# Kernel optimization log

Measured on AMD Instinct MI355X. Metric: run time of the kernel, lower is better.

The kernel has to match this reference:

```python
import jax, jax.numpy as jnp
import numpy as np

LABEL_SMOOTHING = 0.1


def setup_inputs() -> dict:
    key = jax.random.key(0)
    k1, k2, k3 = jax.random.split(key, 3)
    B, N, D = 16384, 1000, 1000  # code structurally requires D == n_classes == N
    inputs = jax.random.uniform(k1, (B, D), dtype=jnp.float32)
    labels = jax.random.randint(k2, (B,), 0, N, dtype=jnp.int64)
    code_book = jax.random.uniform(k3, (N, D), dtype=jnp.float32)
    return {"inputs": inputs, "labels": labels, "code_book": code_book}


def reference(inputs, labels, code_book):
    # inputs: [B, D], code_book: [N, D], D == N (n_classes)
    n_classes = inputs.shape[1]
    # soft targets with label smoothing (same as scatter_ + smoothing)
    soft_target = jax.nn.one_hot(labels, n_classes, dtype=inputs.dtype)
    soft_target = soft_target * (1.0 - LABEL_SMOOTHING) + LABEL_SMOOTHING / n_classes
    # Hamming similarity: sum_d [o*c + (1-o)*(1-c)]  ==  o@c.T + (1-o)@(1-c).T
    # (algebraic rewrite of the [B, N, D] broadcast in the original; same math)
    similarity = (jnp.einsum("bd,nd->bn", inputs, code_book)
                  + jnp.einsum("bd,nd->bn", 1.0 - inputs, 1.0 - code_book))
    logp = jax.nn.log_softmax(similarity, axis=1)
    return jnp.mean(jnp.sum(-soft_target * logp, axis=1))
```

## Files before the change

kernel.cpp:

```cpp
#include <hip/hip_runtime.h>

typedef __attribute__((ext_vector_type(8))) short bf16x8;
typedef __attribute__((ext_vector_type(4))) float f32x4;

#define AS1 __attribute__((address_space(1)))
#define AS3 __attribute__((address_space(3)))

__device__ static inline void gl2lds16(const void* g, void* l) {
  __builtin_amdgcn_global_load_lds((const AS1 unsigned int*)g, (AS3 unsigned int*)l, 16, 0, 0);
}

__device__ static inline unsigned short f2bf(float x) {
  unsigned int u = __float_as_uint(x);
  unsigned int r = u + 0x7FFFu + ((u >> 16) & 1u);
  return (unsigned short)(r >> 16);
}

__global__ __launch_bounds__(256) void prep_inputs_k(const float* __restrict__ in,
                                                     unsigned short* __restrict__ a) {
  int idx = blockIdx.x * 256 + threadIdx.x;
  int row = idx >> 7;
  int g   = idx & 127;
  union { unsigned short u[8]; uint4 v; } pk;
  if (g < 125) {
    const float4* p = (const float4*)(in + (size_t)row * 1000 + g * 8);
    float4 v0 = p[0], v1 = p[1];
    pk.u[0] = f2bf(2.f * v0.x); pk.u[1] = f2bf(2.f * v0.y);
    pk.u[2] = f2bf(2.f * v0.z); pk.u[3] = f2bf(2.f * v0.w);
    pk.u[4] = f2bf(2.f * v1.x); pk.u[5] = f2bf(2.f * v1.y);
    pk.u[6] = f2bf(2.f * v1.z); pk.u[7] = f2bf(2.f * v1.w);
  } else {
    pk.v = make_uint4(0, 0, 0, 0);
  }
  *(uint4*)(a + ((size_t)row << 10) + (g << 3)) = pk.v;
}

__global__ __launch_bounds__(256) void prep_code_k(const float* __restrict__ cb,
                                                   unsigned short* __restrict__ b,
                                                   float* __restrict__ rowsum) {
  int n = blockIdx.x;
  int t = threadIdx.x;
  float s = 0.f;
#pragma unroll
  for (int j = 0; j < 4; ++j) {
    int c = t + j * 256;
    float v = 0.f;
    if (n < 1000 && c < 1000) v = cb[(size_t)n * 1000 + c];
    s += v;
    b[((size_t)n << 10) + c] = f2bf(v);
  }
  __shared__ float red[256];
  red[t] = s;
  __syncthreads();
  for (int o = 128; o > 0; o >>= 1) {
    if (t < o) red[t] += red[t + o];
    __syncthreads();
  }
  if (t == 0) rowsum[n] = (n < 1000) ? red[0] : 0.f;
}

__global__ __launch_bounds__(256) void fix_labels_k(const int* __restrict__ raw,
                                                    int* __restrict__ labs) {
  __shared__ int nz;
  int t = threadIdx.x;
  if (t == 0) nz = 0;
  __syncthreads();
  if (raw[2 * t + 1] != 0) atomicAdd(&nz, 1);
  __syncthreads();
  bool is64 = (nz < 32);
  int row = blockIdx.x * 256 + t;
  labs[row] = is64 ? raw[2 * row] : raw[row];
}

__global__ __launch_bounds__(256, 2) void coding_loss_k(
    const unsigned short* __restrict__ A,
    const unsigned short* __restrict__ B,
    const float* __restrict__ rowsum,
    const int* __restrict__ labels,
    float* __restrict__ Z,
    float* __restrict__ lin) {
  __shared__ __align__(16) unsigned char lds[24576 + 32768 + 1040];
  unsigned short* Ab0 = (unsigned short*)lds;
  unsigned short* Ab1 = Ab0 + 4096;
  unsigned short* Ab2 = Ab1 + 4096;
  unsigned short* Bb0 = Ab2 + 4096;
  unsigned short* Bb1 = Bb0 + 8192;
  float* zbuf = (float*)(lds + 57344);
  float* lbuf = zbuf + 256;

  const int t    = threadIdx.x;
  const int lane = t & 63;
  const int w    = t >> 6;
  const int wr   = w >> 1;
  const int wc   = w & 1;
  const int g16  = lane >> 4;
  const int c16  = lane & 15;
  const int ct   = blockIdx.x & 3;
  const int rt   = blockIdx.x >> 2;
  const int r0   = rt << 7;
  const int c0   = ct << 8;

  size_t a_src[2]; int a_dst[2];
#pragma unroll
  for (int i = 0; i < 2; ++i) {
    int ch = i * 256 + t, row = ch >> 2;
    int sg = (ch & 3) ^ ((row >> 1) & 3);
    a_src[i] = (size_t)(r0 + row) * 1024 + sg * 8;
    a_dst[i] = ch * 8;
  }
  size_t b_src[4]; int b_dst[4];
#pragma unroll
  for (int i = 0; i < 4; ++i) {
    int ch = i * 256 + t, row = ch >> 2;
    int sg = (ch & 3) ^ ((row >> 1) & 3);
    b_src[i] = (size_t)(c0 + row) * 1024 + sg * 8;
    b_dst[i] = ch * 8;
  }

  int a_eoff[4], b_eoff[8];
#pragma unroll
  for (int mi = 0; mi < 4; ++mi) {
    int ar = wr * 64 + mi * 16 + c16;
    a_eoff[mi] = ar * 32 + ((g16 ^ ((ar >> 1) & 3)) << 3);
  }
#pragma unroll
  for (int ni = 0; ni < 8; ++ni) {
    int br = wc * 128 + ni * 16 + c16;
    b_eoff[ni] = br * 32 + ((g16 ^ ((br >> 1) & 3)) << 3);
  }

  f32x4 acc[4][8];
#pragma unroll
  for (int mi = 0; mi < 4; ++mi)
#pragma unroll
    for (int ni = 0; ni < 8; ++ni) acc[mi][ni] = (f32x4)(0.f);

#define STAGE_A(kk, dst) \
  { _Pragma("unroll") for (int i = 0; i < 2; ++i) gl2lds16(A + a_src[i] + (kk) * 32, (dst) + a_dst[i]); }
#define STAGE_B(kk, dst) \
  { _Pragma("unroll") for (int i = 0; i < 4; ++i) gl2lds16(B + b_src[i] + (kk) * 32, (dst) + b_dst[i]); }
#define COMPUTE(pa, pb)                                                                   \
  {                                                                                       \
    bf16x8 af[4], bf[8];                                                                  \
    _Pragma("unroll") for (int mi = 0; mi < 4; ++mi) af[mi] = *(const bf16x8*)((pa) + a_eoff[mi]); \
    _Pragma("unroll") for (int ni = 0; ni < 8; ++ni) bf[ni] = *(const bf16x8*)((pb) + b_eoff[ni]); \
    _Pragma("unroll") for (int mi = 0; mi < 4; ++mi)                                      \
      _Pragma("unroll") for (int ni = 0; ni < 8; ++ni)                                    \
        acc[mi][ni] = __builtin_amdgcn_mfma_f32_16x16x32_bf16(af[mi], bf[ni], acc[mi][ni], 0, 0, 0); \
  }
#define WAITVM(n) __builtin_amdgcn_s_waitcnt(0xF70 | (n))

  STAGE_A(0, Ab0);
  STAGE_B(0, Bb0);
  STAGE_A(1, Ab1);

  unsigned short *pa_cur = Ab0, *pa_nxt = Ab1, *pa_stg = Ab2;
  unsigned short *pb_cur = Bb0, *pb_stg = Bb1;

#pragma unroll 2
  for (int kc = 0; kc < 30; ++kc) {
    STAGE_B(kc + 1, pb_stg);
    STAGE_A(kc + 2, pa_stg);
    WAITVM(8);
    __builtin_amdgcn_s_barrier();
    COMPUTE(pa_cur, pb_cur);
    __builtin_amdgcn_s_barrier();
    unsigned short* tmp = pa_cur; pa_cur = pa_nxt; pa_nxt = pa_stg; pa_stg = tmp;
    tmp = pb_cur; pb_cur = pb_stg; pb_stg = tmp;
  }
  {
    STAGE_B(31, pb_stg);
    WAITVM(6);
    __builtin_amdgcn_s_barrier();
    COMPUTE(pa_cur, pb_cur);
    __builtin_amdgcn_s_barrier();
    unsigned short* tmp = pa_cur; pa_cur = pa_nxt; pa_nxt = tmp;
    tmp = pb_cur; pb_cur = pb_stg; pb_stg = tmp;
  }
  {
    WAITVM(0);
    __builtin_amdgcn_s_barrier();
    COMPUTE(pa_cur, pb_cur);
  }

  float rs[8]; int colg[8];
#pragma unroll
  for (int ni = 0; ni < 8; ++ni) {
    colg[ni] = c0 + wc * 128 + ni * 16 + c16;
    rs[ni]   = rowsum[colg[ni]];
  }
  float lacc = 0.f;
  float ez[4][4];
#pragma unroll
  for (int mi = 0; mi < 4; ++mi)
#pragma unroll
    for (int r = 0; r < 4; ++r) {
      int labv = labels[r0 + wr * 64 + mi * 16 + g16 * 4 + r];
      float e = 0.f;
#pragma unroll
      for (int ni = 0; ni < 8; ++ni) {
        float S = acc[mi][ni][r] - rs[ni];
        e += __expf(S - 40.f);
        lacc += 1e-4f * S;
        if (colg[ni] == labv) lacc += 0.9f * S;
      }
      ez[mi][r] = e;
    }
#pragma unroll
  for (int d = 1; d < 16; d <<= 1)
#pragma unroll
    for (int mi = 0; mi < 4; ++mi)
#pragma unroll
      for (int r = 0; r < 4; ++r) ez[mi][r] += __shfl_xor(ez[mi][r], d, 64);
  if (c16 == 0) {
#pragma unroll
    for (int mi = 0; mi < 4; ++mi)
#pragma unroll
      for (int r = 0; r < 4; ++r) zbuf[w * 64 + mi * 16 + g16 * 4 + r] = ez[mi][r];
  }
#pragma unroll
  for (int d = 1; d < 64; d <<= 1) lacc += __shfl_xor(lacc, d, 64);
  if (lane == 0) lbuf[w] = lacc;
  __syncthreads();
  if (t < 128) {
    int wrg = t >> 6, lr = t & 63;
    float z = zbuf[(wrg * 2 + 0) * 64 + lr] + zbuf[(wrg * 2 + 1) * 64 + lr];
    Z[ct * 16384 + r0 + t] = z;
  }
  if (t == 0) atomicAdd(lin, lbuf[0] + lbuf[1] + lbuf[2] + lbuf[3]);
#undef STAGE_A
#undef STAGE_B
#undef COMPUTE
#undef WAITVM
}

__global__ __launch_bounds__(256) void finalize_k(const float* __restrict__ Z,
                                                  const float* __restrict__ lin,
                                                  float* __restrict__ out) {
  int t = threadIdx.x;
  int row = blockIdx.x * 256 + t;
  float v = 40.f + logf(Z[row] + Z[16384 + row] + Z[2 * 16384 + row] + Z[3 * 16384 + row]);
#pragma unroll
  for (int d = 1; d < 64; d <<= 1) v += __shfl_xor(v, d, 64);
  __shared__ float s[4];
  if ((t & 63) == 0) s[t >> 6] = v;
  __syncthreads();
  if (t == 0) {
    float tot = s[0] + s[1] + s[2] + s[3];
    if (blockIdx.x == 0) tot -= lin[0];
    atomicAdd(out, tot * (1.f / 16384.f));
  }
}

extern "C" void kernel_launch(void* const* d_in, const int* in_sizes, int n_in,
                              void* d_out, int out_size, void* d_ws, size_t ws_size,
                              hipStream_t stream) {
  const float* inputs = (const float*)d_in[0];
  const int* labraw   = (const int*)d_in[1];
  const float* code   = (const float*)d_in[2];

  unsigned short* a_bf = (unsigned short*)d_ws;
  unsigned short* b_bf = a_bf + (size_t)16384 * 1024;
  float* rowsum        = (float*)(b_bf + (size_t)1024 * 1024);
  float* Z             = rowsum + 1024;
  float* lin           = Z + 4 * 16384;
  int* labs            = (int*)(lin + 1);

  hipMemsetAsync(lin, 0, sizeof(float), stream);
  hipMemsetAsync(d_out, 0, sizeof(float), stream);
  fix_labels_k<<<64, 256, 0, stream>>>(labraw, labs);
  prep_inputs_k<<<8192, 256, 0, stream>>>(inputs, a_bf);
  prep_code_k<<<1024, 256, 0, stream>>>(code, b_bf, rowsum);
  coding_loss_k<<<512, 256, 0, stream>>>(a_bf, b_bf, rowsum, labs, Z, lin);
  finalize_k<<<64, 256, 0, stream>>>(Z, lin, (float*)d_out);
}
```

Before: 148.5 us.

## Merge prep kernels and enlarge GEMM tile to 256x256 with double buffering

The three preprocessing kernels and two memsets are merged into a single launch that dispatches on block index, which cuts launch overhead. The main GEMM tile grows from 128x256 to 256x256 per block, giving 8x8 MFMA accumulators per wave and more operand reuse. The 3-stage A pipeline is replaced by plain double buffering with occupancy 1 and 256 blocks. The risks are higher register pressure, only 256 blocks on a GPU with about 256 CUs leaving no latency hiding across blocks, and a shallower prefetch.

```diff
diff --git a/kernel.cpp b/kernel.cpp
--- a/kernel.cpp
+++ b/kernel.cpp
@@ -16,77 +16,71 @@
   return (unsigned short)(r >> 16);
 }
 
-__global__ __launch_bounds__(256) void prep_inputs_k(const float* __restrict__ in,
-                                                     unsigned short* __restrict__ a) {
-  int idx = blockIdx.x * 256 + threadIdx.x;
-  int row = idx >> 7;
-  int g   = idx & 127;
-  union { unsigned short u[8]; uint4 v; } pk;
-  if (g < 125) {
-    const float4* p = (const float4*)(in + (size_t)row * 1000 + g * 8);
-    float4 v0 = p[0], v1 = p[1];
-    pk.u[0] = f2bf(2.f * v0.x); pk.u[1] = f2bf(2.f * v0.y);
-    pk.u[2] = f2bf(2.f * v0.z); pk.u[3] = f2bf(2.f * v0.w);
-    pk.u[4] = f2bf(2.f * v1.x); pk.u[5] = f2bf(2.f * v1.y);
-    pk.u[6] = f2bf(2.f * v1.z); pk.u[7] = f2bf(2.f * v1.w);
+__global__ __launch_bounds__(256) void prep_all_k(
+    const float* __restrict__ in, const int* __restrict__ labraw,
+    const float* __restrict__ cb, unsigned short* __restrict__ a,
+    unsigned short* __restrict__ b, float* __restrict__ rowsum,
+    int* __restrict__ labs, float* __restrict__ lin, float* __restrict__ out) {
+  const int bx = blockIdx.x, t = threadIdx.x;
+  if (bx < 8192) {
+    int idx = bx * 256 + t;
+    int row = idx >> 7, g = idx & 127;
+    union { unsigned short u[8]; uint4 v; } pk;
+    if (g < 125) {
+      const float4* p = (const float4*)(in + (size_t)row * 1000 + g * 8);
+      float4 v0 = p[0], v1 = p[1];
+      pk.u[0] = f2bf(2.f * v0.x); pk.u[1] = f2bf(2.f * v0.y);
+      pk.u[2] = f2bf(2.f * v0.z); pk.u[3] = f2bf(2.f * v0.w);
+      pk.u[4] = f2bf(2.f * v1.x); pk.u[5] = f2bf(2.f * v1.y);
+      pk.u[6] = f2bf(2.f * v1.z); pk.u[7] = f2bf(2.f * v1.w);
+    } else {
+      pk.v = make_uint4(0, 0, 0, 0);
+    }
+    *(uint4*)(a + ((size_t)row << 10) + (g << 3)) = pk.v;
+  } else if (bx < 9216) {
+    int n = bx - 8192;
+    float s = 0.f;
+#pragma unroll
+    for (int j = 0; j < 4; ++j) {
+      int c = t + j * 256;
+      float v = 0.f;
+      if (n < 1000 && c < 1000) v = cb[(size_t)n * 1000 + c];
+      s += v;
+      b[((size_t)n << 10) + c] = f2bf(v);
+    }
+    __shared__ float red[256];
+    red[t] = s;
+    __syncthreads();
+    for (int o = 128; o > 0; o >>= 1) {
+      if (t < o) red[t] += red[t + o];
+      __syncthreads();
+    }
+    if (t == 0) rowsum[n] = (n < 1000) ? red[0] : 0.f;
   } else {
-    pk.v = make_uint4(0, 0, 0, 0);
-  }
-  *(uint4*)(a + ((size_t)row << 10) + (g << 3)) = pk.v;
-}
-
-__global__ __launch_bounds__(256) void prep_code_k(const float* __restrict__ cb,
-                                                   unsigned short* __restrict__ b,
-                                                   float* __restrict__ rowsum) {
-  int n = blockIdx.x;
-  int t = threadIdx.x;
-  float s = 0.f;
-#pragma unroll
-  for (int j = 0; j < 4; ++j) {
-    int c = t + j * 256;
-    float v = 0.f;
-    if (n < 1000 && c < 1000) v = cb[(size_t)n * 1000 + c];
-    s += v;
-    b[((size_t)n << 10) + c] = f2bf(v);
-  }
-  __shared__ float red[256];
-  red[t] = s;
-  __syncthreads();
-  for (int o = 128; o > 0; o >>= 1) {
-    if (t < o) red[t] += red[t + o];
+    __shared__ int nz;
+    if (t == 0) nz = 0;
     __syncthreads();
-  }
-  if (t == 0) rowsum[n] = (n < 1000) ? red[0] : 0.f;
-}
-
-__global__ __launch_bounds__(256) void fix_labels_k(const int* __restrict__ raw,
-                                                    int* __restrict__ labs) {
-  __shared__ int nz;
-  int t = threadIdx.x;
-  if (t == 0) nz = 0;
-  __syncthreads();
-  if (raw[2 * t + 1] != 0) atomicAdd(&nz, 1);
-  __syncthreads();
-  bool is64 = (nz < 32);
-  int row = blockIdx.x * 256 + t;
-  labs[row] = is64 ? raw[2 * row] : raw[row];
-}
-
-__global__ __launch_bounds__(256, 2) void coding_loss_k(
+    if (labraw[2 * t + 1] != 0) atomicAdd(&nz, 1);
+    __syncthreads();
+    bool is64 = (nz < 32);
+    int row = (bx - 9216) * 256 + t;
+    labs[row] = is64 ? labraw[2 * row] : labraw[row];
+    if (bx == 9216 && t == 0) { lin[0] = 0.f; out[0] = 0.f; }
+  }
+}
+
+__global__ __launch_bounds__(256, 1) void coding_loss_k(
     const unsigned short* __restrict__ A,
     const unsigned short* __restrict__ B,
     const float* __restrict__ rowsum,
     const int* __restrict__ labels,
     float* __restrict__ Z,
     float* __restrict__ lin) {
-  __shared__ __align__(16) unsigned char lds[24576 + 32768 + 1040];
-  unsigned short* Ab0 = (unsigned short*)lds;
-  unsigned short* Ab1 = Ab0 + 4096;
-  unsigned short* Ab2 = Ab1 + 4096;
-  unsigned short* Bb0 = Ab2 + 4096;
-  unsigned short* Bb1 = Bb0 + 8192;
-  float* zbuf = (float*)(lds + 57344);
-  float* lbuf = zbuf + 256;
+  __shared__ __align__(16) unsigned short lds[32768];
+  unsigned short* Ab0 = lds;
+  unsigned short* Ab1 = lds + 8192;
+  unsigned short* Bb0 = lds + 16384;
+  unsigned short* Bb1 = lds + 24576;
 
   const int t    = threadIdx.x;
   const int lane = t & 63;
@@ -97,141 +91,110 @@
   const int c16  = lane & 15;
   const int ct   = blockIdx.x & 3;
   const int rt   = blockIdx.x >> 2;
-  const int r0   = rt << 7;
+  const int r0   = rt << 8;
   const int c0   = ct << 8;
 
-  size_t a_src[2]; int a_dst[2];
-#pragma unroll
-  for (int i = 0; i < 2; ++i) {
+  size_t a_src[4], b_src[4]; int dstoff[4];
+#pragma unroll
+  for (int i = 0; i < 4; ++i) {
     int ch = i * 256 + t, row = ch >> 2;
     int sg = (ch & 3) ^ ((row >> 1) & 3);
     a_src[i] = (size_t)(r0 + row) * 1024 + sg * 8;
-    a_dst[i] = ch * 8;
-  }
-  size_t b_src[4]; int b_dst[4];
-#pragma unroll
-  for (int i = 0; i < 4; ++i) {
-    int ch = i * 256 + t, row = ch >> 2;
-    int sg = (ch & 3) ^ ((row >> 1) & 3);
     b_src[i] = (size_t)(c0 + row) * 1024 + sg * 8;
-    b_dst[i] = ch * 8;
-  }
-
-  int a_eoff[4], b_eoff[8];
-#pragma unroll
-  for (int mi = 0; mi < 4; ++mi) {
-    int ar = wr * 64 + mi * 16 + c16;
-    a_eoff[mi] = ar * 32 + ((g16 ^ ((ar >> 1) & 3)) << 3);
-  }
-#pragma unroll
-  for (int ni = 0; ni < 8; ++ni) {
-    int br = wc * 128 + ni * 16 + c16;
-    b_eoff[ni] = br * 32 + ((g16 ^ ((br >> 1) & 3)) << 3);
-  }
-
-  f32x4 acc[4][8];
-#pragma unroll
-  for (int mi = 0; mi < 4; ++mi)
+    dstoff[i] = ch * 8;
+  }
+  int a_eoff[8], b_eoff[8];
+#pragma unroll
+  for (int i = 0; i < 8; ++i) {
+    int ar = wr * 128 + i * 16 + c16;
+    a_eoff[i] = ar * 32 + ((g16 ^ ((ar >> 1) & 3)) << 3);
+    int br = wc * 128 + i * 16 + c16;
+    b_eoff[i] = br * 32 + ((g16 ^ ((br >> 1) & 3)) << 3);
+  }
+
+  f32x4 acc[8][8];
+#pragma unroll
+  for (int mi = 0; mi < 8; ++mi)
 #pragma unroll
     for (int ni = 0; ni < 8; ++ni) acc[mi][ni] = (f32x4)(0.f);
 
 #define STAGE_A(kk, dst) \
-  { _Pragma("unroll") for (int i = 0; i < 2; ++i) gl2lds16(A + a_src[i] + (kk) * 32, (dst) + a_dst[i]); }
+  { _Pragma("unroll") for (int i = 0; i < 4; ++i) gl2lds16(A + a_src[i] + (kk) * 32, (dst) + dstoff[i]); }
 #define STAGE_B(kk, dst) \
-  { _Pragma("unroll") for (int i = 0; i < 4; ++i) gl2lds16(B + b_src[i] + (kk) * 32, (dst) + b_dst[i]); }
+  { _Pragma("unroll") for (int i = 0; i < 4; ++i) gl2lds16(B + b_src[i] + (kk) * 32, (dst) + dstoff[i]); }
 #define COMPUTE(pa, pb)                                                                   \
   {                                                                                       \
-    bf16x8 af[4], bf[8];                                                                  \
-    _Pragma("unroll") for (int mi = 0; mi < 4; ++mi) af[mi] = *(const bf16x8*)((pa) + a_eoff[mi]); \
-    _Pragma("unroll") for (int ni = 0; ni < 8; ++ni) bf[ni] = *(const bf16x8*)((pb) + b_eoff[ni]); \
-    _Pragma("unroll") for (int mi = 0; mi < 4; ++mi)                                      \
+    bf16x8 af[8], bf[8];                                                                  \
+    _Pragma("unroll") for (int i = 0; i < 8; ++i) af[i] = *(const bf16x8*)((pa) + a_eoff[i]); \
+    _Pragma("unroll") for (int i = 0; i < 8; ++i) bf[i] = *(const bf16x8*)((pb) + b_eoff[i]); \
+    _Pragma("unroll") for (int mi = 0; mi < 8; ++mi)                                      \
       _Pragma("unroll") for (int ni = 0; ni < 8; ++ni)                                    \
         acc[mi][ni] = __builtin_amdgcn_mfma_f32_16x16x32_bf16(af[mi], bf[ni], acc[mi][ni], 0, 0, 0); \
   }
-#define WAITVM(n) __builtin_amdgcn_s_waitcnt(0xF70 | (n))
 
   STAGE_A(0, Ab0);
   STAGE_B(0, Bb0);
-  STAGE_A(1, Ab1);
-
-  unsigned short *pa_cur = Ab0, *pa_nxt = Ab1, *pa_stg = Ab2;
-  unsigned short *pb_cur = Bb0, *pb_stg = Bb1;
+  unsigned short *pa = Ab0, *pan = Ab1, *pb = Bb0, *pbn = Bb1;
 
 #pragma unroll 2
-  for (int kc = 0; kc < 30; ++kc) {
-    STAGE_B(kc + 1, pb_stg);
-    STAGE_A(kc + 2, pa_stg);
-    WAITVM(8);
+  for (int J = 0; J < 31; ++J) {
+    STAGE_A(J + 1, pan);
+    STAGE_B(J + 1, pbn);
+    __builtin_amdgcn_s_waitcnt(0xF78);
     __builtin_amdgcn_s_barrier();
-    COMPUTE(pa_cur, pb_cur);
+    COMPUTE(pa, pb);
     __builtin_amdgcn_s_barrier();
-    unsigned short* tmp = pa_cur; pa_cur = pa_nxt; pa_nxt = pa_stg; pa_stg = tmp;
-    tmp = pb_cur; pb_cur = pb_stg; pb_stg = tmp;
-  }
-  {
-    STAGE_B(31, pb_stg);
-    WAITVM(6);
-    __builtin_amdgcn_s_barrier();
-    COMPUTE(pa_cur, pb_cur);
-    __builtin_amdgcn_s_barrier();
-    unsigned short* tmp = pa_cur; pa_cur = pa_nxt; pa_nxt = tmp;
-    tmp = pb_cur; pb_cur = pb_stg; pb_stg = tmp;
-  }
-  {
-    WAITVM(0);
-    __builtin_amdgcn_s_barrier();
-    COMPUTE(pa_cur, pb_cur);
-  }
-
-  float rs[8]; int colg[8];
+    unsigned short* x = pa; pa = pan; pan = x;
+    x = pb; pb = pbn; pbn = x;
+  }
+  __builtin_amdgcn_s_waitcnt(0xF70);
+  __builtin_amdgcn_s_barrier();
+  COMPUTE(pa, pb);
+  __syncthreads();
+
+  float* zbuf = (float*)lds;
+  float* lbuf = zbuf + 512;
+  float rs[8]; int gcol[8];
 #pragma unroll
   for (int ni = 0; ni < 8; ++ni) {
-    colg[ni] = c0 + wc * 128 + ni * 16 + c16;
-    rs[ni]   = rowsum[colg[ni]];
+    gcol[ni] = c0 + wc * 128 + ni * 16 + c16;
+    rs[ni]   = rowsum[gcol[ni]];
   }
   float lacc = 0.f;
-  float ez[4][4];
-#pragma unroll
-  for (int mi = 0; mi < 4; ++mi)
+#pragma unroll
+  for (int mi = 0; mi < 8; ++mi) {
 #pragma unroll
     for (int r = 0; r < 4; ++r) {
-      int labv = labels[r0 + wr * 64 + mi * 16 + g16 * 4 + r];
+      int lrow = mi * 16 + g16 * 4 + r;
+      int labv = labels[r0 + wr * 128 + lrow];
       float e = 0.f;
 #pragma unroll
       for (int ni = 0; ni < 8; ++ni) {
         float S = acc[mi][ni][r] - rs[ni];
         e += __expf(S - 40.f);
         lacc += 1e-4f * S;
-        if (colg[ni] == labv) lacc += 0.9f * S;
+        if (gcol[ni] == labv) lacc += 0.9f * S;
       }
-      ez[mi][r] = e;
-    }
-#pragma unroll
-  for (int d = 1; d < 16; d <<= 1)
-#pragma unroll
-    for (int mi = 0; mi < 4; ++mi)
-#pragma unroll
-      for (int r = 0; r < 4; ++r) ez[mi][r] += __shfl_xor(ez[mi][r], d, 64);
-  if (c16 == 0) {
-#pragma unroll
-    for (int mi = 0; mi < 4; ++mi)
-#pragma unroll
-      for (int r = 0; r < 4; ++r) zbuf[w * 64 + mi * 16 + g16 * 4 + r] = ez[mi][r];
+      e += __shfl_xor(e, 1, 64);
+      e += __shfl_xor(e, 2, 64);
+      e += __shfl_xor(e, 4, 64);
+      e += __shfl_xor(e, 8, 64);
+      if (c16 == 0) zbuf[w * 128 + lrow] = e;
+    }
   }
 #pragma unroll
   for (int d = 1; d < 64; d <<= 1) lacc += __shfl_xor(lacc, d, 64);
   if (lane == 0) lbuf[w] = lacc;
   __syncthreads();
-  if (t < 128) {
-    int wrg = t >> 6, lr = t & 63;
-    float z = zbuf[(wrg * 2 + 0) * 64 + lr] + zbuf[(wrg * 2 + 1) * 64 + lr];
+  {
+    int wrg = t >> 7, l7 = t & 127;
+    float z = zbuf[(wrg * 2 + 0) * 128 + l7] + zbuf[(wrg * 2 + 1) * 128 + l7];
     Z[ct * 16384 + r0 + t] = z;
   }
   if (t == 0) atomicAdd(lin, lbuf[0] + lbuf[1] + lbuf[2] + lbuf[3]);
 #undef STAGE_A
 #undef STAGE_B
 #undef COMPUTE
-#undef WAITVM
 }
 
 __global__ __launch_bounds__(256) void finalize_k(const float* __restrict__ Z,
@@ -266,11 +229,8 @@
   float* lin           = Z + 4 * 16384;
   int* labs            = (int*)(lin + 1);
 
-  hipMemsetAsync(lin, 0, sizeof(float), stream);
-  hipMemsetAsync(d_out, 0, sizeof(float), stream);
-  fix_labels_k<<<64, 256, 0, stream>>>(labraw, labs);
-  prep_inputs_k<<<8192, 256, 0, stream>>>(inputs, a_bf);
-  prep_code_k<<<1024, 256, 0, stream>>>(code, b_bf, rowsum);
-  coding_loss_k<<<512, 256, 0, stream>>>(a_bf, b_bf, rowsum, labs, Z, lin);
+  prep_all_k<<<9280, 256, 0, stream>>>(inputs, labraw, code, a_bf, b_bf, rowsum,
+                                       labs, lin, (float*)d_out);
+  coding_loss_k<<<256, 256, 0, stream>>>(a_bf, b_bf, rowsum, labs, Z, lin);
   finalize_k<<<64, 256, 0, stream>>>(Z, lin, (float*)d_out);
 }
```

Result: faster. 145.4 us (-2.0%).
